# Kernel optimization log

Measured on AMD Instinct MI355X. Metric: run time of the kernel, lower is better.

Reference implementation:

```python
import jax, jax.numpy as jnp
import numpy as np

B, S, D, E, K = 2, 4096, 1024, 8, 2

def setup_inputs() -> dict:
    key = jax.random.key(0)
    k1, k2, k3, k4, k5 = jax.random.split(key, 5)
    x = jax.random.normal(k1, (B, S, D), dtype=jnp.float32)
    expert_weights = jax.random.uniform(k2, (B, S, K), dtype=jnp.float32)
    top_k_indices = jax.random.randint(k3, (B, S, K), 0, E, dtype=jnp.int32)
    W = jax.random.normal(k4, (E, D, D), dtype=jnp.float32) * (1.0 / np.sqrt(D))
    b = jax.random.normal(k5, (E, D), dtype=jnp.float32) * 0.01
    return {"x": x, "expert_weights": expert_weights,
            "top_k_indices": top_k_indices, "W": W, "b": b}

def reference(x, expert_weights, top_k_indices, W, b):
    # Dense all-expert linear: [B,S,E,Dout]
    expert_outputs = jnp.einsum('bsd,edf->bsef', x, W) + b  # bias broadcasts over b,s
    # Gather the top-k expert outputs per token: [B,S,K,Dout]
    gathered = jnp.take_along_axis(expert_outputs, top_k_indices[:, :, :, None], axis=2)
    # Weighted combine over k
    output = jnp.sum(expert_weights[:, :, :, None] * gathered, axis=2)
    return output
```

## Files before the change

### kernel.cpp

```cpp
#include <hip/hip_runtime.h>
#include <hip/hip_bf16.h>
#include <cstdio>
#include <cstdint>

static constexpr int TOK = 8192;
static constexpr int DIM = 1024;
static constexpr int NEXP = 8;
static constexpr int NGRP = 16;

typedef unsigned short u16;
typedef unsigned int u32;

using floatx4 = __attribute__((ext_vector_type(4))) float;
using bf16x8  = __attribute__((ext_vector_type(8))) __bf16;


__device__ __forceinline__ u16 f2bf(float f) {
  union { float f; u32 u; } v; v.f = f;
  u32 r = v.u + 0x7fffu + ((v.u >> 16) & 1u);
  return (u16)(r >> 16);
}

__device__ __forceinline__ float bf2f(u16 b) {
  union { u32 u; float f; } v; v.u = (u32)b << 16;
  return v.f;
}

__device__ __forceinline__ void gload_lds16(const void* g, void* l) {
  __builtin_amdgcn_global_load_lds(
      (const __attribute__((address_space(1))) void*)g,
      (__attribute__((address_space(3))) void*)l,
      16, 0, 0);
}

__global__ __launch_bounds__(1024)
void prep_kernel(const int* __restrict__ idx, const float* __restrict__ ew,
                 int* __restrict__ meta, int* __restrict__ tileMap,
                 int* __restrict__ tokList, float* __restrict__ wList,
                 int* __restrict__ posOf) {
  __shared__ int cnt[NGRP], offS[NGRP], cur[NGRP], tbase[NGRP];
  const int tid = threadIdx.x;
  if (tid < NGRP) cnt[tid] = 0;
  __syncthreads();
  int gl[16];
#pragma unroll
  for (int j = 0; j < 16; ++j) {
    int i = tid + 1024 * j;
    int g = ((i & 1) << 3) | idx[i];
    gl[j] = g;
    atomicAdd(&cnt[g], 1);
  }
  __syncthreads();
  if (tid == 0) {
    int run = 0, t = 0, tk0 = 0;
    for (int g = 0; g < NGRP; ++g) {
      offS[g] = run; cur[g] = run; tbase[g] = t;
      t += (cnt[g] + 127) >> 7;
      if (g == NEXP - 1) tk0 = t;
      run += cnt[g];
    }
    meta[48] = t;
    meta[49] = tk0;
  }
  __syncthreads();
  if (tid < NGRP) {
    meta[tid] = cnt[tid];
    meta[16 + tid] = offS[tid];
    int b = tbase[tid], n = (cnt[tid] + 127) >> 7;
    for (int m0 = 0; m0 < n; ++m0) tileMap[b + m0] = (tid << 12) | m0;
  }
#pragma unroll
  for (int j = 0; j < 16; ++j) {
    int i = tid + 1024 * j;
    int pos = atomicAdd(&cur[gl[j]], 1);
    tokList[pos] = i >> 1;
    wList[pos] = ew[i];
    posOf[i] = pos;
  }
}

__global__ __launch_bounds__(256)
void setup_kernel(const float* __restrict__ x, const int* __restrict__ posOf,
                  u16* __restrict__ Abuf, const float* __restrict__ W,
                  u16* __restrict__ wt) {
  const int bid = blockIdx.x;
  const int tid = threadIdx.x;
  if (bid < TOK) {
    const int t = bid;
    float4 v = reinterpret_cast<const float4*>(x + ((size_t)t << 10))[tid];
    ushort4 o;
    o.x = f2bf(v.x); o.y = f2bf(v.y); o.z = f2bf(v.z); o.w = f2bf(v.w);
    const int p0 = posOf[2 * t], p1 = posOf[2 * t + 1];
    reinterpret_cast<ushort4*>(Abuf + ((size_t)p0 << 10))[tid] = o;
    reinterpret_cast<ushort4*>(Abuf + ((size_t)p1 << 10))[tid] = o;
  } else {
    __shared__ u16 tile[32][33];
    const int b = bid - TOK;
    const int e = b >> 10;
    const int f0 = ((b >> 5) & 31) * 32, d0 = (b & 31) * 32;
    const float* src = W + ((size_t)e << 20);
    u16* dst = wt + ((size_t)e << 20);
    const int tx = tid & 31, ty = tid >> 5;
#pragma unroll
    for (int j = 0; j < 4; ++j) {
      int d = d0 + ty + 8 * j;
      tile[ty + 8 * j][tx] = f2bf(src[(size_t)d * DIM + f0 + tx]);
    }
    __syncthreads();
#pragma unroll
    for (int j = 0; j < 4; ++j) {
      int f = f0 + ty + 8 * j;
      dst[(size_t)f * DIM + d0 + tx] = tile[tx][ty + 8 * j];
    }
  }
}

__global__ __launch_bounds__(256, 4)
void moe_gemm_kernel(const u16* __restrict__ Abuf, const u16* __restrict__ wt,
                     const float* __restrict__ bias, const int* __restrict__ tokList,
                     const float* __restrict__ wList, const int* __restrict__ meta,
                     const int* __restrict__ tileMap, float* __restrict__ out,
                     u16* __restrict__ cbuf, int pass) {
  constexpr int BM = 128, BN = 128, BK = 64;
  const int chunk = gridDim.y;
  int lin = blockIdx.y * 8 + blockIdx.x;
  int swz = (lin & 7) * chunk + (lin >> 3);
  int tileIdx = swz >> 3, nt = swz & 7;

  int tBase = 0, tEnd = meta[48];
  const int tilesK0 = meta[49];
  if (pass == 0) tEnd = tilesK0;
  else if (pass == 1) tBase = tilesK0;
  tileIdx += tBase;
  if (tileIdx >= tEnd) return;

  const int tm = tileMap[tileIdx];
  const int g = tm >> 12, m0 = tm & 0xfff;
  const int e = g & (NEXP - 1);
  const int nrem = meta[g] - m0 * BM;
  const int listBase = meta[16 + g] + m0 * BM;

  __shared__ __align__(16) u16 As[BM * BK];
  __shared__ __align__(16) u16 Bs[BN * BK];

  const int tid = threadIdx.x;
  const int rowA = tid >> 3;
  const int chnk = tid & 7;
  const int csw  = chnk ^ (rowA & 7);
  const u16* wb = wt + ((size_t)e << 20);
  const u16* ab = Abuf + ((size_t)listBase << 10);

  const int wid = tid >> 6, lane = tid & 63;
  const int wm = (wid >> 1) * 64, wn = (wid & 1) * 64;
  const int lr = lane & 15, lg = lane >> 4;
  const int rx = lr & 7;

  floatx4 acc[4][4];
#pragma unroll
  for (int i = 0; i < 4; ++i)
#pragma unroll
    for (int j = 0; j < 4; ++j) acc[i][j] = (floatx4){0.f, 0.f, 0.f, 0.f};

  for (int kt = 0; kt < DIM / BK; ++kt) {
    __syncthreads();
#pragma unroll
    for (int r = 0; r < 4; ++r) {
      const int row = rowA + 32 * r;
      gload_lds16(ab + ((size_t)row << 10) + kt * BK + csw * 8,
                  &As[row * BK + chnk * 8]);
    }
#pragma unroll
    for (int r = 0; r < 4; ++r) {
      const int row = rowA + 32 * r;
      gload_lds16(wb + ((size_t)(nt * BN + row) << 10) + kt * BK + csw * 8,
                  &Bs[row * BK + chnk * 8]);
    }
    asm volatile("s_waitcnt vmcnt(0)" ::: "memory");
    __syncthreads();

#pragma unroll
    for (int ks = 0; ks < 2; ++ks) {
      bf16x8 av[4], bv[4];
#pragma unroll
      for (int mi = 0; mi < 4; ++mi)
        av[mi] = *reinterpret_cast<const bf16x8*>(
            &As[(wm + mi * 16 + lr) * BK + (((ks * 4 + lg) ^ rx)) * 8]);
#pragma unroll
      for (int ni = 0; ni < 4; ++ni)
        bv[ni] = *reinterpret_cast<const bf16x8*>(
            &Bs[(wn + ni * 16 + lr) * BK + (((ks * 4 + lg) ^ rx)) * 8]);
#pragma unroll
      for (int mi = 0; mi < 4; ++mi)
#pragma unroll
        for (int ni = 0; ni < 4; ++ni)
          acc[mi][ni] = __builtin_amdgcn_mfma_f32_16x16x32_bf16(av[mi], bv[ni], acc[mi][ni], 0, 0, 0);
    }
  }

  const bool toCbuf = (pass < 0) && (g >= NEXP);
  const bool rmw = (pass == 1);
  const float* bp = bias + e * DIM;
#pragma unroll
  for (int mi = 0; mi < 4; ++mi) {
#pragma unroll
    for (int r = 0; r < 4; ++r) {
      const int rl = wm + mi * 16 + lg * 4 + r;
      if (rl < nrem) {
        const int   tok = tokList[listBase + rl];
        const float w   = wList[listBase + rl];
        const size_t rowOff = (size_t)tok << 10;
#pragma unroll
        for (int ni = 0; ni < 4; ++ni) {
          const int col = nt * BN + wn + ni * 16 + lr;
          const float v = w * (acc[mi][ni][r] + bp[col]);
          if (toCbuf)      cbuf[rowOff + col] = f2bf(v);
          else if (rmw)    out[rowOff + col] += v;
          else             out[rowOff + col] = v;
        }
      }
    }
  }
}

__global__ __launch_bounds__(256)
void combine_kernel(float* __restrict__ out, const u16* __restrict__ cbuf) {
  const int p = blockIdx.x * 256 + threadIdx.x;
  uint4 c = reinterpret_cast<const uint4*>(cbuf)[p];
  float4* o4 = reinterpret_cast<float4*>(out) + 2 * (size_t)p;
  float4 a = o4[0], b = o4[1];
  a.x += bf2f((u16)(c.x & 0xffff)); a.y += bf2f((u16)(c.x >> 16));
  a.z += bf2f((u16)(c.y & 0xffff)); a.w += bf2f((u16)(c.y >> 16));
  b.x += bf2f((u16)(c.z & 0xffff)); b.y += bf2f((u16)(c.z >> 16));
  b.z += bf2f((u16)(c.w & 0xffff)); b.w += bf2f((u16)(c.w >> 16));
  o4[0] = a; o4[1] = b;
}

extern "C" void kernel_launch(void* const* d_in, const int* in_sizes, int n_in,
                              void* d_out, int out_size, void* d_ws, size_t ws_size,
                              hipStream_t stream) {
  const float* x    = (const float*)d_in[0];
  const float* ew   = (const float*)d_in[1];
  const int*   idx  = (const int*)d_in[2];
  const float* W    = (const float*)d_in[3];
  const float* bias = (const float*)d_in[4];
  float* out = (float*)d_out;

  char* ws = (char*)d_ws;
  u16*   Abuf = (u16*)ws;
  u16*   wtp  = (u16*)(ws + ((size_t)32 << 20));
  u16*   cbuf = (u16*)(ws + ((size_t)48 << 20));

  const size_t needB = ((size_t)48 << 20) + (194 << 10);
  const size_t needA = ((size_t)64 << 20) + (194 << 10);
  if (ws_size < needB) {
    fprintf(stderr, "kernel_launch: ws_size %zu < needed %zu\n", ws_size, needB);
    return;
  }
  const bool modeA = (ws_size >= needA);
  char* tail = ws + (modeA ? ((size_t)64 << 20) : ((size_t)48 << 20));
  int*   tokList = (int*)tail;
  float* wList   = (float*)(tail + (64 << 10));
  int*   posOf   = (int*)(tail + (128 << 10));
  int*   meta    = (int*)(tail + (192 << 10));
  int*   tileMap = (int*)(tail + (193 << 10));

  prep_kernel<<<1, 1024, 0, stream>>>(idx, ew, meta, tileMap, tokList, wList, posOf);
  setup_kernel<<<TOK + 8192, 256, 0, stream>>>(x, posOf, Abuf, W, wtp);

  if (modeA) {
    moe_gemm_kernel<<<dim3(8, 144), 256, 0, stream>>>(
        Abuf, wtp, bias, tokList, wList, meta, tileMap, out, cbuf, -1);
    combine_kernel<<<TOK * DIM / 8 / 256, 256, 0, stream>>>(out, cbuf);
  } else {
    moe_gemm_kernel<<<dim3(8, 72), 256, 0, stream>>>(
        Abuf, wtp, bias, tokList, wList, meta, tileMap, out, nullptr, 0);
    moe_gemm_kernel<<<dim3(8, 72), 256, 0, stream>>>(
        Abuf, wtp, bias, tokList, wList, meta, tileMap, out, nullptr, 1);
  }
}
```

Measured before the change: 118.9 us.

## Privatize prep histogram per wave and write both k-slots to bf16 buffers

The prep kernel now keeps a separate histogram and scatter cursor per wave instead of one shared set, which reduces LDS atomic contention in the single-block routing kernel. When the workspace is large enough, a new mode sends both top-k slot outputs as bf16 to two scratch buffers. A combine kernel then sums them and writes the output without reading fp32 out back. This replaces a fp32 read-modify-write of the output with an extra bf16 buffer write, at the cost of rounding the slot-0 contributions to bf16 as well.

```diff
diff --git a/kernel.cpp b/kernel.cpp
--- a/kernel.cpp
+++ b/kernel.cpp
@@ -38,9 +38,12 @@
                  int* __restrict__ meta, int* __restrict__ tileMap,
                  int* __restrict__ tokList, float* __restrict__ wList,
                  int* __restrict__ posOf) {
-  __shared__ int cnt[NGRP], offS[NGRP], cur[NGRP], tbase[NGRP];
+  __shared__ int cnt2[16][NGRP];
+  __shared__ int cur2[16][NGRP];
+  __shared__ int tot[NGRP], offS[NGRP], tbase[NGRP];
   const int tid = threadIdx.x;
-  if (tid < NGRP) cnt[tid] = 0;
+  const int wid = tid >> 6;
+  if (tid < 16 * NGRP) ((int*)cnt2)[tid] = 0;
   __syncthreads();
   int gl[16];
 #pragma unroll
@@ -48,31 +51,42 @@
     int i = tid + 1024 * j;
     int g = ((i & 1) << 3) | idx[i];
     gl[j] = g;
-    atomicAdd(&cnt[g], 1);
+    atomicAdd(&cnt2[wid][g], 1);
+  }
+  __syncthreads();
+  if (tid < NGRP) {
+    int s = 0;
+    for (int w = 0; w < 16; ++w) { cur2[w][tid] = s; s += cnt2[w][tid]; }
+    tot[tid] = s;
   }
   __syncthreads();
   if (tid == 0) {
     int run = 0, t = 0, tk0 = 0;
     for (int g = 0; g < NGRP; ++g) {
-      offS[g] = run; cur[g] = run; tbase[g] = t;
-      t += (cnt[g] + 127) >> 7;
+      offS[g] = run; tbase[g] = t;
+      t += (tot[g] + 127) >> 7;
       if (g == NEXP - 1) tk0 = t;
-      run += cnt[g];
+      run += tot[g];
     }
     meta[48] = t;
     meta[49] = tk0;
   }
   __syncthreads();
   if (tid < NGRP) {
-    meta[tid] = cnt[tid];
+    meta[tid] = tot[tid];
     meta[16 + tid] = offS[tid];
-    int b = tbase[tid], n = (cnt[tid] + 127) >> 7;
+    int b = tbase[tid], n = (tot[tid] + 127) >> 7;
     for (int m0 = 0; m0 < n; ++m0) tileMap[b + m0] = (tid << 12) | m0;
   }
+  if (tid < 16 * NGRP) {
+    int w = tid >> 4, g = tid & 15;
+    cur2[w][g] += offS[g];
+  }
+  __syncthreads();
 #pragma unroll
   for (int j = 0; j < 16; ++j) {
     int i = tid + 1024 * j;
-    int pos = atomicAdd(&cur[gl[j]], 1);
+    int pos = atomicAdd(&cur2[wid][gl[j]], 1);
     tokList[pos] = i >> 1;
     wList[pos] = ew[i];
     posOf[i] = pos;
@@ -120,7 +134,8 @@
                      const float* __restrict__ bias, const int* __restrict__ tokList,
                      const float* __restrict__ wList, const int* __restrict__ meta,
                      const int* __restrict__ tileMap, float* __restrict__ out,
-                     u16* __restrict__ cbuf, int pass) {
+                     u16* __restrict__ cbufA, u16* __restrict__ cbufB, int mode,
+                     int pass) {
   constexpr int BM = 128, BN = 128, BK = 64;
   const int chunk = gridDim.y;
   int lin = blockIdx.y * 8 + blockIdx.x;
@@ -129,8 +144,7 @@
 
   int tBase = 0, tEnd = meta[48];
   const int tilesK0 = meta[49];
-  if (pass == 0) tEnd = tilesK0;
-  else if (pass == 1) tBase = tilesK0;
+  if (mode == 0) { if (pass == 0) tEnd = tilesK0; else tBase = tilesK0; }
   tileIdx += tBase;
   if (tileIdx >= tEnd) return;
 
@@ -197,8 +211,11 @@
     }
   }
 
-  const bool toCbuf = (pass < 0) && (g >= NEXP);
-  const bool rmw = (pass == 1);
+  u16* cb = nullptr;
+  bool rmw = false, f32out = false;
+  if (mode == 2)      cb = (g < NEXP) ? cbufA : cbufB;
+  else if (mode == 1) { if (g < NEXP) f32out = true; else cb = cbufA; }
+  else                { f32out = true; rmw = (pass == 1); }
   const float* bp = bias + e * DIM;
 #pragma unroll
   for (int mi = 0; mi < 4; ++mi) {
@@ -213,13 +230,31 @@
         for (int ni = 0; ni < 4; ++ni) {
           const int col = nt * BN + wn + ni * 16 + lr;
           const float v = w * (acc[mi][ni][r] + bp[col]);
-          if (toCbuf)      cbuf[rowOff + col] = f2bf(v);
-          else if (rmw)    out[rowOff + col] += v;
-          else             out[rowOff + col] = v;
+          if (f32out) { if (rmw) out[rowOff + col] += v; else out[rowOff + col] = v; }
+          else        cb[rowOff + col] = f2bf(v);
         }
       }
     }
   }
+}
+
+__global__ __launch_bounds__(256)
+void combine2_kernel(float* __restrict__ out, const u16* __restrict__ cbufA,
+                     const u16* __restrict__ cbufB) {
+  const int p = blockIdx.x * 256 + threadIdx.x;
+  uint4 ca = reinterpret_cast<const uint4*>(cbufA)[p];
+  uint4 cb = reinterpret_cast<const uint4*>(cbufB)[p];
+  float4 r0, r1;
+  r0.x = bf2f((u16)(ca.x & 0xffff)) + bf2f((u16)(cb.x & 0xffff));
+  r0.y = bf2f((u16)(ca.x >> 16))    + bf2f((u16)(cb.x >> 16));
+  r0.z = bf2f((u16)(ca.y & 0xffff)) + bf2f((u16)(cb.y & 0xffff));
+  r0.w = bf2f((u16)(ca.y >> 16))    + bf2f((u16)(cb.y >> 16));
+  r1.x = bf2f((u16)(ca.z & 0xffff)) + bf2f((u16)(cb.z & 0xffff));
+  r1.y = bf2f((u16)(ca.z >> 16))    + bf2f((u16)(cb.z >> 16));
+  r1.z = bf2f((u16)(ca.w & 0xffff)) + bf2f((u16)(cb.w & 0xffff));
+  r1.w = bf2f((u16)(ca.w >> 16))    + bf2f((u16)(cb.w >> 16));
+  float4* o4 = reinterpret_cast<float4*>(out) + 2 * (size_t)p;
+  o4[0] = r0; o4[1] = r1;
 }
 
 __global__ __launch_bounds__(256)
@@ -246,18 +281,23 @@
   float* out = (float*)d_out;
 
   char* ws = (char*)d_ws;
-  u16*   Abuf = (u16*)ws;
-  u16*   wtp  = (u16*)(ws + ((size_t)32 << 20));
-  u16*   cbuf = (u16*)(ws + ((size_t)48 << 20));
-
-  const size_t needB = ((size_t)48 << 20) + (194 << 10);
-  const size_t needA = ((size_t)64 << 20) + (194 << 10);
-  if (ws_size < needB) {
-    fprintf(stderr, "kernel_launch: ws_size %zu < needed %zu\n", ws_size, needB);
+  u16*   Abuf  = (u16*)ws;
+  u16*   wtp   = (u16*)(ws + ((size_t)32 << 20));
+  u16*   cbufA = (u16*)(ws + ((size_t)48 << 20));
+  u16*   cbufB = (u16*)(ws + ((size_t)64 << 20));
+
+  const size_t tailSz = (size_t)(194 << 10);
+  const size_t need0 = ((size_t)48 << 20) + tailSz;
+  const size_t need1 = ((size_t)64 << 20) + tailSz;
+  const size_t need2 = ((size_t)80 << 20) + tailSz;
+  if (ws_size < need0) {
+    fprintf(stderr, "kernel_launch: ws_size %zu < needed %zu\n", ws_size, need0);
     return;
   }
-  const bool modeA = (ws_size >= needA);
-  char* tail = ws + (modeA ? ((size_t)64 << 20) : ((size_t)48 << 20));
+  const int mode = (ws_size >= need2) ? 2 : (ws_size >= need1) ? 1 : 0;
+  char* tail = ws + ((mode == 2) ? ((size_t)80 << 20)
+                                 : (mode == 1) ? ((size_t)64 << 20)
+                                               : ((size_t)48 << 20));
   int*   tokList = (int*)tail;
   float* wList   = (float*)(tail + (64 << 10));
   int*   posOf   = (int*)(tail + (128 << 10));
@@ -267,14 +307,18 @@
   prep_kernel<<<1, 1024, 0, stream>>>(idx, ew, meta, tileMap, tokList, wList, posOf);
   setup_kernel<<<TOK + 8192, 256, 0, stream>>>(x, posOf, Abuf, W, wtp);
 
-  if (modeA) {
+  if (mode == 2) {
     moe_gemm_kernel<<<dim3(8, 144), 256, 0, stream>>>(
-        Abuf, wtp, bias, tokList, wList, meta, tileMap, out, cbuf, -1);
-    combine_kernel<<<TOK * DIM / 8 / 256, 256, 0, stream>>>(out, cbuf);
+        Abuf, wtp, bias, tokList, wList, meta, tileMap, out, cbufA, cbufB, 2, 0);
+    combine2_kernel<<<TOK * DIM / 8 / 256, 256, 0, stream>>>(out, cbufA, cbufB);
+  } else if (mode == 1) {
+    moe_gemm_kernel<<<dim3(8, 144), 256, 0, stream>>>(
+        Abuf, wtp, bias, tokList, wList, meta, tileMap, out, cbufA, nullptr, 1, 0);
+    combine_kernel<<<TOK * DIM / 8 / 256, 256, 0, stream>>>(out, cbufA);
   } else {
     moe_gemm_kernel<<<dim3(8, 72), 256, 0, stream>>>(
-        Abuf, wtp, bias, tokList, wList, meta, tileMap, out, nullptr, 0);
+        Abuf, wtp, bias, tokList, wList, meta, tileMap, out, nullptr, nullptr, 0, 0);
     moe_gemm_kernel<<<dim3(8, 72), 256, 0, stream>>>(
-        Abuf, wtp, bias, tokList, wList, meta, tileMap, out, nullptr, 1);
-  }
-}
+        Abuf, wtp, bias, tokList, wList, meta, tileMap, out, nullptr, nullptr, 0, 1);
+  }
+}
```

New measurement: 116.5 us. 1.02x faster.
